# Kernel optimization log

Hardware: AMD Instinct MI355X
Metric: run time of the kernel (lower is better)

## Reference

```python
import jax, jax.numpy as jnp
import numpy as np

B, T, C = 2, 2048, 1024
E, K = 8, 2            # n_experts, top_k (n_experts_active)
H = 2736               # round8(int(4*C*2/3)) SwiGLU hidden dim


def setup_inputs() -> dict:
    key = jax.random.key(0)
    ks = jax.random.split(key, 8)
    def w(k, shape, fan_in):
        return jax.random.normal(k, shape, jnp.float32) * (1.0 / np.sqrt(fan_in))
    x = jax.random.normal(ks[0], (B, T, C), jnp.float32)
    router_w = w(ks[1], (C, E), C)          # gate.weight.T
    wg = w(ks[2], (E, C, H), C)             # stacked expert w_gate.weight.T
    wu = w(ks[3], (E, C, H), C)             # stacked expert w_up.weight.T
    wd = w(ks[4], (E, H, C), H)             # stacked expert w_down.weight.T
    sg = w(ks[5], (C, H), C)                # shared expert gate
    su = w(ks[6], (C, H), C)                # shared expert up
    sd = w(ks[7], (H, C), H)                # shared expert down
    return {"x": x, "router_w": router_w, "wg": wg, "wu": wu, "wd": wd,
            "sg": sg, "su": su, "sd": sd}


def reference(x, router_w, wg, wu, wd, sg, su, sd):
    Bx, Tx, Cx = x.shape
    xf = x.reshape(-1, Cx)                       # (Tk, C)
    Tk = xf.shape[0]

    # --- router ---
    logits = xf @ router_w                       # (Tk, E)
    top_v, top_i = jax.lax.top_k(logits, K)      # (Tk, K)
    rw = jax.nn.softmax(top_v, axis=-1)          # normalized weights over selected

    # combine weights per (token, expert): scatter router weights
    rows = jnp.arange(Tk)[:, None]
    w_te = jnp.zeros((Tk, E), xf.dtype).at[rows, top_i].add(rw)   # (Tk, E)

    # --- experts (dense dispatch; weight w_te zeros out unselected experts) ---
    gate = jnp.einsum('tc,ech->teh', xf, wg)     # (Tk, E, H)
    up = jnp.einsum('tc,ech->teh', xf, wu)
    h = jax.nn.silu(gate) * up                   # SwiGLU hidden
    out = jnp.einsum('teh,te,ehc->tc', h, w_te, wd)   # weighted combine

    # --- shared expert ---
    out = out + (jax.nn.silu(xf @ sg) * (xf @ su)) @ sd

    # --- aux load-balancing loss ---
    mask = jnp.zeros((Tk, E), xf.dtype).at[rows, top_i].add(1.0)
    f = mask.mean(axis=0) / K
    p = jax.nn.softmax(logits, axis=-1).mean(axis=0)
    aux_loss = E * (f * p).sum()

    return out.reshape(Bx, Tx, Cx), aux_loss
```

## Files before the change

kernel.cpp:

```cpp
#include <hip/hip_runtime.h>

typedef _Float16 f16;
typedef _Float16 f16x4 __attribute__((ext_vector_type(4)));
typedef _Float16 f16x8 __attribute__((ext_vector_type(8)));
typedef float f32x4 __attribute__((ext_vector_type(4)));

#define TK 4096
#define CD 1024
#define HD 2736
#define HP 2816
#define MT 104
#define RC 13312

#define GLDS16(ldsp, gp) __builtin_amdgcn_global_load_lds( \
    (const __attribute__((address_space(1))) unsigned int*)(gp), \
    (__attribute__((address_space(3))) unsigned int*)(ldsp), 16, 0, 0)

static constexpr size_t WS_XB  = 0;
static constexpr size_t WS_H   = WS_XB  + (size_t)TK*CD*2;
static constexpr size_t WS_WGT = WS_H   + (size_t)RC*HP*2;
static constexpr size_t WS_WUT = WS_WGT + (size_t)8*HP*CD*2;
static constexpr size_t WS_WDT = WS_WUT + (size_t)8*HP*CD*2;
static constexpr size_t WS_SGT = WS_WDT + (size_t)8*CD*HP*2;
static constexpr size_t WS_SUT = WS_SGT + (size_t)HP*CD*2;
static constexpr size_t WS_SDT = WS_SUT + (size_t)HP*CD*2;
static constexpr size_t WS_CT  = WS_SDT + (size_t)CD*HP*2;
static constexpr size_t WS_OBUF = WS_WGT;
static constexpr size_t CT_STOK = 0;
static constexpr size_t CT_SW   = CT_STOK + (size_t)RC*4;
static constexpr size_t CT_TI   = CT_SW   + (size_t)RC*4;
static constexpr size_t CT_TW   = CT_TI   + (size_t)TK*2*4;
static constexpr size_t CT_ISL  = CT_TW   + (size_t)TK*2*4;
static constexpr size_t CT_CNT  = CT_ISL  + (size_t)TK*2*4;
static constexpr size_t CT_PS   = CT_CNT  + 32;
static constexpr size_t CT_CUR  = CT_PS   + 32;
static constexpr size_t CT_OFF  = CT_CUR  + 32;
static constexpr size_t CT_SIZE = CT_OFF  + 64;

__global__ __launch_bounds__(256) void k_tr(
    const float* __restrict__ srcMain, f16* __restrict__ dstMain,
    const float* __restrict__ srcSh,   f16* __restrict__ dstSh,
    int R, int Cc, int Rp, int Cp, int nMain,
    size_t sstride, size_t dstride) {
    const float* src; f16* dst;
    if ((int)blockIdx.z < nMain) {
        src = srcMain + (size_t)blockIdx.z * sstride;
        dst = dstMain + (size_t)blockIdx.z * dstride;
    } else {
        src = srcSh; dst = dstSh;
    }
    const int tid = threadIdx.x;
    const int l = tid & 63, w = tid >> 6;
    const int cc0 = blockIdx.x * 128 + w * 32 + (l >> 3) * 4;
    const int rr0 = blockIdx.y * 64 + (l & 7) * 8;
    float4 v[8];
    #pragma unroll
    for (int e = 0; e < 8; e++) {
        int gr = rr0 + e;
        if (gr < R && cc0 + 3 < Cc) {
            v[e] = *(const float4*)(src + (size_t)gr * Cc + cc0);
        } else {
            float* ve = (float*)&v[e];
            #pragma unroll
            for (int c = 0; c < 4; c++)
                ve[c] = (gr < R && cc0 + c < Cc) ? src[(size_t)gr * Cc + cc0 + c] : 0.f;
        }
    }
    #pragma unroll
    for (int c = 0; c < 4; c++) {
        const float* vp = (const float*)v;
        f16x8 o = { (f16)vp[0*4+c], (f16)vp[1*4+c], (f16)vp[2*4+c], (f16)vp[3*4+c],
                    (f16)vp[4*4+c], (f16)vp[5*4+c], (f16)vp[6*4+c], (f16)vp[7*4+c] };
        *(f16x8*)(dst + (size_t)(cc0 + c) * Rp + rr0) = o;
    }
}

__global__ void k_router(const float* __restrict__ x, const float* __restrict__ rw,
                         f16* __restrict__ xb,
                         int* __restrict__ topi, float* __restrict__ topw,
                         int* __restrict__ cnt, float* __restrict__ psum) {
    __shared__ float pl[8];
    int tid = threadIdx.x;
    if (tid < 8) pl[tid] = 0.f;
    __syncthreads();
    int wave = tid >> 6, lane = tid & 63;
    int t = blockIdx.x * 4 + wave;
    float acc[8];
    #pragma unroll
    for (int e = 0; e < 8; e++) acc[e] = 0.f;
    const float* xr = x + (size_t)t * CD;
    f16* xbr = xb + (size_t)t * CD;
    for (int i = 0; i < CD / 64; i++) {
        int c = lane + i * 64;
        float xv = xr[c];
        xbr[c] = (f16)xv;
        const float* wr = rw + c * 8;
        #pragma unroll
        for (int e = 0; e < 8; e++) acc[e] = fmaf(xv, wr[e], acc[e]);
    }
    #pragma unroll
    for (int e = 0; e < 8; e++) {
        #pragma unroll
        for (int off = 32; off; off >>= 1) acc[e] += __shfl_xor(acc[e], off);
    }
    if (lane == 0) {
        float v1 = -1e30f; int i1 = 0;
        #pragma unroll
        for (int e = 0; e < 8; e++) if (acc[e] > v1) { v1 = acc[e]; i1 = e; }
        float v2 = -1e30f; int i2 = (i1 == 0) ? 1 : 0;
        #pragma unroll
        for (int e = 0; e < 8; e++) if (e != i1 && acc[e] > v2) { v2 = acc[e]; i2 = e; }
        float b = expf(v2 - v1);
        float w1 = 1.f / (1.f + b);
        topi[t*2] = i1; topi[t*2+1] = i2;
        topw[t*2] = w1; topw[t*2+1] = b * w1;
        atomicAdd(&cnt[i1], 1);
        atomicAdd(&cnt[i2], 1);
        float m = acc[0];
        #pragma unroll
        for (int e = 1; e < 8; e++) m = fmaxf(m, acc[e]);
        float pe[8]; float s = 0.f;
        #pragma unroll
        for (int e = 0; e < 8; e++) { pe[e] = expf(acc[e] - m); s += pe[e]; }
        float inv = 1.f / s;
        #pragma unroll
        for (int e = 0; e < 8; e++) atomicAdd(&pl[e], pe[e] * inv);
    }
    __syncthreads();
    if (tid < 8) atomicAdd(&psum[tid], pl[tid]);
}

__global__ void k_prefix(const int* __restrict__ cnt, int* __restrict__ cur,
                         int* __restrict__ offs) {
    if (threadIdx.x == 0 && blockIdx.x == 0) {
        int off = 0;
        for (int e = 0; e < 8; e++) {
            offs[e] = off; cur[e] = off;
            off += (cnt[e] + 127) & ~127;
        }
        offs[8] = off;
        offs[9] = RC;
    }
}

__global__ void k_scatter(const int* __restrict__ topi, const float* __restrict__ topw,
                          int* __restrict__ cur, const int* __restrict__ offs,
                          int* __restrict__ stok, float* __restrict__ sw,
                          int* __restrict__ islot) {
    int t = blockIdx.x * 256 + threadIdx.x;
    if (t >= TK) return;
    #pragma unroll
    for (int s = 0; s < 2; s++) {
        int e = topi[t*2 + s];
        int pos = atomicAdd(&cur[e], 1);
        stok[pos] = t;
        sw[pos] = topw[t*2 + s];
        islot[t*2 + s] = pos;
    }
    int base = offs[8];
    stok[base + t] = t;
    sw[base + t] = 1.0f;
}

__global__ __launch_bounds__(256, 2) void k_ffn1(
    const f16* __restrict__ xb, const f16* __restrict__ wgt,
    const f16* __restrict__ wut, const f16* __restrict__ sgt,
    const f16* __restrict__ sut, const int* __restrict__ offs,
    const int* __restrict__ cnt, const int* __restrict__ stok,
    f16* __restrict__ hbuf)
{
    __shared__ f16 As[128*64];
    __shared__ f16 Bg[128*64];
    __shared__ f16 Bu[128*64];

    const int n0 = blockIdx.x * 128;
    const int m0 = blockIdx.y * 128;
    int g = 0;
    while (g < 8 && m0 >= offs[g+1]) g++;
    if (m0 >= offs[8] + TK) return;
    if (g < 8 && (m0 - offs[g]) >= cnt[g]) return;

    const f16* __restrict__ Wg = (g < 8) ? wgt + (size_t)g * HP * CD : sgt;
    const f16* __restrict__ Wu = (g < 8) ? wut + (size_t)g * HP * CD : sut;

    const int tid = threadIdx.x;
    const int lane = tid & 63;
    const int w = tid >> 6;
    const int w32 = w * 32;

    const int asw = (((lane & 7) ^ (lane >> 3)) << 3);
    int rA[4];
    #pragma unroll
    for (int i = 0; i < 4; i++)
        rA[i] = stok[m0 + w32 + 8*i + (lane >> 3)] * CD + asw;
    const int rB = (n0 + w32 + (lane >> 3)) * CD + asw;

    f32x4 accg[4][4], accu[4][4];
    #pragma unroll
    for (int i = 0; i < 4; i++)
        #pragma unroll
        for (int j = 0; j < 4; j++)
            #pragma unroll
            for (int r = 0; r < 4; r++) { accg[i][j][r] = 0.f; accu[i][j][r] = 0.f; }

    const int wm = (w >> 1) * 64;
    const int wn = (w & 1) * 64;
    const int fm = lane & 15;
    const int fq = lane >> 4;
    const int fs = fm & 7;

    for (int k0 = 0; k0 < CD; k0 += 64) {
        #pragma unroll
        for (int i = 0; i < 4; i++) {
            GLDS16(&As[(w32 + 8*i) * 64], xb + rA[i] + k0);
            GLDS16(&Bg[(w32 + 8*i) * 64], Wg + rB + i*8*CD + k0);
            GLDS16(&Bu[(w32 + 8*i) * 64], Wu + rB + i*8*CD + k0);
        }
        __syncthreads();
        #pragma unroll
        for (int kk = 0; kk < 2; kk++) {
            const int sw = ((((kk << 2) | fq) ^ fs) << 3);
            f16x8 af[4];
            #pragma unroll
            for (int mi = 0; mi < 4; mi++)
                af[mi] = *(const f16x8*)&As[(wm + mi*16 + fm) * 64 + sw];
            #pragma unroll
            for (int ni = 0; ni < 4; ni++) {
                f16x8 bgf = *(const f16x8*)&Bg[(wn + ni*16 + fm) * 64 + sw];
                f16x8 bur = *(const f16x8*)&Bu[(wn + ni*16 + fm) * 64 + sw];
                #pragma unroll
                for (int mi = 0; mi < 4; mi++) {
                    accg[mi][ni] = __builtin_amdgcn_mfma_f32_16x16x32_f16(af[mi], bgf, accg[mi][ni], 0, 0, 0);
                    accu[mi][ni] = __builtin_amdgcn_mfma_f32_16x16x32_f16(af[mi], bur, accu[mi][ni], 0, 0, 0);
                }
            }
        }
        __syncthreads();
    }

    #pragma unroll
    for (int mi = 0; mi < 4; mi++) {
        #pragma unroll
        for (int ni = 0; ni < 4; ni++) {
            #pragma unroll
            for (int r = 0; r < 4; r++) {
                int row = m0 + wm + mi*16 + fq*4 + r;
                int col = n0 + wn + ni*16 + fm;
                float gv = accg[mi][ni][r];
                float uv = accu[mi][ni][r];
                float hv = gv / (1.f + __expf(-gv)) * uv;
                hbuf[(size_t)row * HP + col] = (f16)hv;
            }
        }
    }
}

__global__ __launch_bounds__(256, 2) void k_ffn2(
    const f16* __restrict__ hbuf, const f16* __restrict__ wdt,
    const f16* __restrict__ sdt, const int* __restrict__ offs,
    const int* __restrict__ cnt, float* __restrict__ obuf)
{
    __shared__ f16 As[128*64];
    __shared__ f16 Bs[128*64];

    const int n0 = blockIdx.x * 128;
    const int m0 = blockIdx.y * 128;
    int g = 0;
    while (g < 8 && m0 >= offs[g+1]) g++;
    if (m0 >= offs[8] + TK) return;
    if (g < 8 && (m0 - offs[g]) >= cnt[g]) return;
    const f16* __restrict__ W = (g < 8) ? wdt + (size_t)g * CD * HP : sdt;

    const int tid = threadIdx.x;
    const int lane = tid & 63;
    const int w = tid >> 6;
    const int w32 = w * 32;

    const int asw = (((lane & 7) ^ (lane >> 3)) << 3);
    const int rA = (m0 + w32 + (lane >> 3)) * HP + asw;
    const int rB = (n0 + w32 + (lane >> 3)) * HP + asw;

    f32x4 acc[4][4];
    #pragma unroll
    for (int i = 0; i < 4; i++)
        #pragma unroll
        for (int j = 0; j < 4; j++)
            #pragma unroll
            for (int r = 0; r < 4; r++) acc[i][j][r] = 0.f;

    const int wm = (w >> 1) * 64;
    const int wn = (w & 1) * 64;
    const int fm = lane & 15;
    const int fq = lane >> 4;
    const int fs = fm & 7;

    for (int k0 = 0; k0 < HP; k0 += 64) {
        #pragma unroll
        for (int i = 0; i < 4; i++) {
            GLDS16(&As[(w32 + 8*i) * 64], hbuf + (size_t)rA + i*8*HP + k0);
            GLDS16(&Bs[(w32 + 8*i) * 64], W    + (size_t)rB + i*8*HP + k0);
        }
        __syncthreads();
        #pragma unroll
        for (int kk = 0; kk < 2; kk++) {
            const int sw = ((((kk << 2) | fq) ^ fs) << 3);
            f16x8 af[4];
            #pragma unroll
            for (int mi = 0; mi < 4; mi++)
                af[mi] = *(const f16x8*)&As[(wm + mi*16 + fm) * 64 + sw];
            #pragma unroll
            for (int ni = 0; ni < 4; ni++) {
                f16x8 bfr = *(const f16x8*)&Bs[(wn + ni*16 + fm) * 64 + sw];
                #pragma unroll
                for (int mi = 0; mi < 4; mi++)
                    acc[mi][ni] = __builtin_amdgcn_mfma_f32_16x16x32_f16(af[mi], bfr, acc[mi][ni], 0, 0, 0);
            }
        }
        __syncthreads();
    }

    #pragma unroll
    for (int mi = 0; mi < 4; mi++) {
        #pragma unroll
        for (int r = 0; r < 4; r++) {
            int row = m0 + wm + mi*16 + fq*4 + r;
            #pragma unroll
            for (int ni = 0; ni < 4; ni++) {
                int col = n0 + wn + ni*16 + fm;
                obuf[(size_t)row * CD + col] = acc[mi][ni][r];
            }
        }
    }
}

__global__ __launch_bounds__(256) void k_comb(
    const float* __restrict__ obuf, const int* __restrict__ islot,
    const float* __restrict__ topw, const int* __restrict__ offs,
    float* __restrict__ out)
{
    const int t = blockIdx.x;
    const int c = threadIdx.x * 4;
    const int s0 = islot[t*2], s1 = islot[t*2+1];
    const float w0 = topw[t*2], w1 = topw[t*2+1];
    const int sh = offs[8] + t;
    float4 a = *(const float4*)(obuf + (size_t)s0 * CD + c);
    float4 b = *(const float4*)(obuf + (size_t)s1 * CD + c);
    float4 s = *(const float4*)(obuf + (size_t)sh * CD + c);
    float4 o;
    o.x = fmaf(w0, a.x, fmaf(w1, b.x, s.x));
    o.y = fmaf(w0, a.y, fmaf(w1, b.y, s.y));
    o.z = fmaf(w0, a.z, fmaf(w1, b.z, s.z));
    o.w = fmaf(w0, a.w, fmaf(w1, b.w, s.w));
    *(float4*)(out + (size_t)t * CD + c) = o;
}

__global__ void k_aux(const int* __restrict__ cnt, const float* __restrict__ psum,
                      float* __restrict__ out_aux) {
    if (threadIdx.x == 0 && blockIdx.x == 0) {
        float a = 0.f;
        for (int e = 0; e < 8; e++) {
            float f = (float)cnt[e] / ((float)TK * 2.f);
            float p = psum[e] / (float)TK;
            a += f * p;
        }
        out_aux[0] = 8.f * a;
    }
}

extern "C" void kernel_launch(void* const* d_in, const int* in_sizes, int n_in,
                              void* d_out, int out_size, void* d_ws, size_t ws_size,
                              hipStream_t stream) {
    const float* x  = (const float*)d_in[0];
    const float* rw = (const float*)d_in[1];
    const float* wg = (const float*)d_in[2];
    const float* wu = (const float*)d_in[3];
    const float* wd = (const float*)d_in[4];
    const float* sg = (const float*)d_in[5];
    const float* su = (const float*)d_in[6];
    const float* sd = (const float*)d_in[7];
    float* out = (float*)d_out;

    char* ws = (char*)d_ws;
    f16* xb   = (f16*)(ws + WS_XB);
    f16* hbuf = (f16*)(ws + WS_H);
    f16* wgt  = (f16*)(ws + WS_WGT);
    f16* wut  = (f16*)(ws + WS_WUT);
    f16* wdt  = (f16*)(ws + WS_WDT);
    f16* sgt  = (f16*)(ws + WS_SGT);
    f16* sut  = (f16*)(ws + WS_SUT);
    f16* sdt  = (f16*)(ws + WS_SDT);
    float* obuf = (float*)(ws + WS_OBUF);
    char* ct  = ws + WS_CT;
    int*   stok = (int*)  (ct + CT_STOK);
    float* swt  = (float*)(ct + CT_SW);
    int*   topi = (int*)  (ct + CT_TI);
    float* topw = (float*)(ct + CT_TW);
    int*   isl  = (int*)  (ct + CT_ISL);
    int*   cnt  = (int*)  (ct + CT_CNT);
    float* psum = (float*)(ct + CT_PS);
    int*   cur  = (int*)  (ct + CT_CUR);
    int*   offs = (int*)  (ct + CT_OFF);

    hipMemsetAsync(ct, 0, CT_SIZE, stream);

    k_router<<<dim3(TK / 4), dim3(256), 0, stream>>>(x, rw, xb, topi, topw, cnt, psum);
    k_prefix<<<dim3(1), dim3(64), 0, stream>>>(cnt, cur, offs);
    k_scatter<<<dim3(TK / 256), dim3(256), 0, stream>>>(topi, topw, cur, offs, stok, swt, isl);

    k_tr<<<dim3(HP/128, CD/64, 9), dim3(256), 0, stream>>>(
        wg, wgt, sg, sgt, CD, HD, CD, HP, 8, (size_t)CD*HD, (size_t)HP*CD);
    k_tr<<<dim3(HP/128, CD/64, 9), dim3(256), 0, stream>>>(
        wu, wut, su, sut, CD, HD, CD, HP, 8, (size_t)CD*HD, (size_t)HP*CD);
    k_tr<<<dim3(CD/128, HP/64, 9), dim3(256), 0, stream>>>(
        wd, wdt, sd, sdt, HD, CD, HP, CD, 8, (size_t)HD*CD, (size_t)CD*HP);

    k_ffn1<<<dim3(HP/128, MT), dim3(256), 0, stream>>>(xb, wgt, wut, sgt, sut, offs, cnt, stok, hbuf);
    k_ffn2<<<dim3(CD/128, MT), dim3(256), 0, stream>>>(hbuf, wdt, sdt, offs, cnt, obuf);
    k_comb<<<dim3(TK), dim3(256), 0, stream>>>(obuf, isl, topw, offs, out);
    k_aux<<<dim3(1), dim3(64), 0, stream>>>(cnt, psum, out + (size_t)TK * CD);
}
```

Before: 774.2 us.

## Fuse combine into FFN2 via atomics, merge transposes, remap workgroups, raise occupancy

The down-projection kernel now scales each row by its router weight and atomically adds it into the zeroed output. This removes the intermediate fp32 buffer and the separate combine kernel. The gate and up weight transposes are merged into one launch. Both FFN kernels remap workgroup IDs with an XCD-style interleave and raise launch-bounds occupancy hints. The costs are atomic contention on fp32 output rows (three contributions per token), an extra memset of the output, and possible register spills from the higher occupancy targets.

```diff
diff --git a/kernel.cpp b/kernel.cpp
--- a/kernel.cpp
+++ b/kernel.cpp
@@ -25,7 +25,6 @@
 static constexpr size_t WS_SUT = WS_SGT + (size_t)HP*CD*2;
 static constexpr size_t WS_SDT = WS_SUT + (size_t)HP*CD*2;
 static constexpr size_t WS_CT  = WS_SDT + (size_t)CD*HP*2;
-static constexpr size_t WS_OBUF = WS_WGT;
 static constexpr size_t CT_STOK = 0;
 static constexpr size_t CT_SW   = CT_STOK + (size_t)RC*4;
 static constexpr size_t CT_TI   = CT_SW   + (size_t)RC*4;
@@ -37,11 +36,58 @@
 static constexpr size_t CT_OFF  = CT_CUR  + 32;
 static constexpr size_t CT_SIZE = CT_OFF  + 64;
 
+__device__ __forceinline__ void tr_body(const float* __restrict__ src,
+                                        f16* __restrict__ dst,
+                                        int R, int Cc, int Rp) {
+    const int tid = threadIdx.x;
+    const int l = tid & 63, w = tid >> 6;
+    const int cc0 = blockIdx.x * 128 + w * 32 + (l >> 3) * 4;
+    const int rr0 = blockIdx.y * 64 + (l & 7) * 8;
+    float4 v[8];
+    #pragma unroll
+    for (int e = 0; e < 8; e++) {
+        int gr = rr0 + e;
+        if (gr < R && cc0 + 3 < Cc) {
+            v[e] = *(const float4*)(src + (size_t)gr * Cc + cc0);
+        } else {
+            float* ve = (float*)&v[e];
+            #pragma unroll
+            for (int c = 0; c < 4; c++)
+                ve[c] = (gr < R && cc0 + c < Cc) ? src[(size_t)gr * Cc + cc0 + c] : 0.f;
+        }
+    }
+    #pragma unroll
+    for (int c = 0; c < 4; c++) {
+        const float* vp = (const float*)v;
+        f16x8 o = { (f16)vp[0*4+c], (f16)vp[1*4+c], (f16)vp[2*4+c], (f16)vp[3*4+c],
+                    (f16)vp[4*4+c], (f16)vp[5*4+c], (f16)vp[6*4+c], (f16)vp[7*4+c] };
+        *(f16x8*)(dst + (size_t)(cc0 + c) * Rp + rr0) = o;
+    }
+}
+
+__global__ __launch_bounds__(256) void k_tr2(
+    const float* __restrict__ wg, f16* __restrict__ wgt,
+    const float* __restrict__ sg, f16* __restrict__ sgt,
+    const float* __restrict__ wu, f16* __restrict__ wut,
+    const float* __restrict__ su, f16* __restrict__ sut,
+    int R, int Cc, int Rp, size_t sstride, size_t dstride) {
+    const int z = blockIdx.z;
+    const float* src; f16* dst;
+    if (z < 9) {
+        if (z < 8) { src = wg + (size_t)z * sstride; dst = wgt + (size_t)z * dstride; }
+        else       { src = sg; dst = sgt; }
+    } else {
+        int z2 = z - 9;
+        if (z2 < 8) { src = wu + (size_t)z2 * sstride; dst = wut + (size_t)z2 * dstride; }
+        else        { src = su; dst = sut; }
+    }
+    tr_body(src, dst, R, Cc, Rp);
+}
+
 __global__ __launch_bounds__(256) void k_tr(
     const float* __restrict__ srcMain, f16* __restrict__ dstMain,
     const float* __restrict__ srcSh,   f16* __restrict__ dstSh,
-    int R, int Cc, int Rp, int Cp, int nMain,
-    size_t sstride, size_t dstride) {
+    int R, int Cc, int Rp, int nMain, size_t sstride, size_t dstride) {
     const float* src; f16* dst;
     if ((int)blockIdx.z < nMain) {
         src = srcMain + (size_t)blockIdx.z * sstride;
@@ -49,30 +95,7 @@
     } else {
         src = srcSh; dst = dstSh;
     }
-    const int tid = threadIdx.x;
-    const int l = tid & 63, w = tid >> 6;
-    const int cc0 = blockIdx.x * 128 + w * 32 + (l >> 3) * 4;
-    const int rr0 = blockIdx.y * 64 + (l & 7) * 8;
-    float4 v[8];
-    #pragma unroll
-    for (int e = 0; e < 8; e++) {
-        int gr = rr0 + e;
-        if (gr < R && cc0 + 3 < Cc) {
-            v[e] = *(const float4*)(src + (size_t)gr * Cc + cc0);
-        } else {
-            float* ve = (float*)&v[e];
-            #pragma unroll
-            for (int c = 0; c < 4; c++)
-                ve[c] = (gr < R && cc0 + c < Cc) ? src[(size_t)gr * Cc + cc0 + c] : 0.f;
-        }
-    }
-    #pragma unroll
-    for (int c = 0; c < 4; c++) {
-        const float* vp = (const float*)v;
-        f16x8 o = { (f16)vp[0*4+c], (f16)vp[1*4+c], (f16)vp[2*4+c], (f16)vp[3*4+c],
-                    (f16)vp[4*4+c], (f16)vp[5*4+c], (f16)vp[6*4+c], (f16)vp[7*4+c] };
-        *(f16x8*)(dst + (size_t)(cc0 + c) * Rp + rr0) = o;
-    }
+    tr_body(src, dst, R, Cc, Rp);
 }
 
 __global__ void k_router(const float* __restrict__ x, const float* __restrict__ rw,
@@ -145,8 +168,7 @@
 
 __global__ void k_scatter(const int* __restrict__ topi, const float* __restrict__ topw,
                           int* __restrict__ cur, const int* __restrict__ offs,
-                          int* __restrict__ stok, float* __restrict__ sw,
-                          int* __restrict__ islot) {
+                          int* __restrict__ stok, float* __restrict__ sw) {
     int t = blockIdx.x * 256 + threadIdx.x;
     if (t >= TK) return;
     #pragma unroll
@@ -155,14 +177,13 @@
         int pos = atomicAdd(&cur[e], 1);
         stok[pos] = t;
         sw[pos] = topw[t*2 + s];
-        islot[t*2 + s] = pos;
     }
     int base = offs[8];
     stok[base + t] = t;
     sw[base + t] = 1.0f;
 }
 
-__global__ __launch_bounds__(256, 2) void k_ffn1(
+__global__ __launch_bounds__(256, 3) void k_ffn1(
     const f16* __restrict__ xb, const f16* __restrict__ wgt,
     const f16* __restrict__ wut, const f16* __restrict__ sgt,
     const f16* __restrict__ sut, const int* __restrict__ offs,
@@ -173,8 +194,12 @@
     __shared__ f16 Bg[128*64];
     __shared__ f16 Bu[128*64];
 
-    const int n0 = blockIdx.x * 128;
-    const int m0 = blockIdx.y * 128;
+    const int flat = blockIdx.y * gridDim.x + blockIdx.x;
+    const int nwg  = gridDim.x * gridDim.y;
+    const int wgid = (flat & 7) * (nwg >> 3) + (flat >> 3);
+    const int n0 = (wgid % gridDim.x) * 128;
+    const int m0 = (wgid / gridDim.x) * 128;
+
     int g = 0;
     while (g < 8 && m0 >= offs[g+1]) g++;
     if (m0 >= offs[8] + TK) return;
@@ -255,16 +280,21 @@
     }
 }
 
-__global__ __launch_bounds__(256, 2) void k_ffn2(
+__global__ __launch_bounds__(256, 4) void k_ffn2(
     const f16* __restrict__ hbuf, const f16* __restrict__ wdt,
     const f16* __restrict__ sdt, const int* __restrict__ offs,
-    const int* __restrict__ cnt, float* __restrict__ obuf)
+    const int* __restrict__ cnt, const int* __restrict__ stok,
+    const float* __restrict__ swt, float* __restrict__ out)
 {
     __shared__ f16 As[128*64];
     __shared__ f16 Bs[128*64];
 
-    const int n0 = blockIdx.x * 128;
-    const int m0 = blockIdx.y * 128;
+    const int flat = blockIdx.y * gridDim.x + blockIdx.x;
+    const int nwg  = gridDim.x * gridDim.y;
+    const int wgid = (flat & 7) * (nwg >> 3) + (flat >> 3);
+    const int n0 = (wgid % gridDim.x) * 128;
+    const int m0 = (wgid / gridDim.x) * 128;
+
     int g = 0;
     while (g < 8 && m0 >= offs[g+1]) g++;
     if (m0 >= offs[8] + TK) return;
@@ -324,34 +354,16 @@
         #pragma unroll
         for (int r = 0; r < 4; r++) {
             int row = m0 + wm + mi*16 + fq*4 + r;
+            int t = stok[row];
+            float rowW = swt[row];
+            float* orow = out + (size_t)t * CD + n0;
             #pragma unroll
             for (int ni = 0; ni < 4; ni++) {
-                int col = n0 + wn + ni*16 + fm;
-                obuf[(size_t)row * CD + col] = acc[mi][ni][r];
+                int col = wn + ni*16 + fm;
+                atomicAdd(orow + col, rowW * acc[mi][ni][r]);
             }
         }
     }
-}
-
-__global__ __launch_bounds__(256) void k_comb(
-    const float* __restrict__ obuf, const int* __restrict__ islot,
-    const float* __restrict__ topw, const int* __restrict__ offs,
-    float* __restrict__ out)
-{
-    const int t = blockIdx.x;
-    const int c = threadIdx.x * 4;
-    const int s0 = islot[t*2], s1 = islot[t*2+1];
-    const float w0 = topw[t*2], w1 = topw[t*2+1];
-    const int sh = offs[8] + t;
-    float4 a = *(const float4*)(obuf + (size_t)s0 * CD + c);
-    float4 b = *(const float4*)(obuf + (size_t)s1 * CD + c);
-    float4 s = *(const float4*)(obuf + (size_t)sh * CD + c);
-    float4 o;
-    o.x = fmaf(w0, a.x, fmaf(w1, b.x, s.x));
-    o.y = fmaf(w0, a.y, fmaf(w1, b.y, s.y));
-    o.z = fmaf(w0, a.z, fmaf(w1, b.z, s.z));
-    o.w = fmaf(w0, a.w, fmaf(w1, b.w, s.w));
-    *(float4*)(out + (size_t)t * CD + c) = o;
 }
 
 __global__ void k_aux(const int* __restrict__ cnt, const float* __restrict__ psum,
@@ -389,33 +401,29 @@
     f16* sgt  = (f16*)(ws + WS_SGT);
     f16* sut  = (f16*)(ws + WS_SUT);
     f16* sdt  = (f16*)(ws + WS_SDT);
-    float* obuf = (float*)(ws + WS_OBUF);
     char* ct  = ws + WS_CT;
     int*   stok = (int*)  (ct + CT_STOK);
     float* swt  = (float*)(ct + CT_SW);
     int*   topi = (int*)  (ct + CT_TI);
     float* topw = (float*)(ct + CT_TW);
-    int*   isl  = (int*)  (ct + CT_ISL);
     int*   cnt  = (int*)  (ct + CT_CNT);
     float* psum = (float*)(ct + CT_PS);
     int*   cur  = (int*)  (ct + CT_CUR);
     int*   offs = (int*)  (ct + CT_OFF);
 
     hipMemsetAsync(ct, 0, CT_SIZE, stream);
+    hipMemsetAsync(out, 0, (size_t)TK * CD * 4, stream);
 
     k_router<<<dim3(TK / 4), dim3(256), 0, stream>>>(x, rw, xb, topi, topw, cnt, psum);
     k_prefix<<<dim3(1), dim3(64), 0, stream>>>(cnt, cur, offs);
-    k_scatter<<<dim3(TK / 256), dim3(256), 0, stream>>>(topi, topw, cur, offs, stok, swt, isl);
-
-    k_tr<<<dim3(HP/128, CD/64, 9), dim3(256), 0, stream>>>(
-        wg, wgt, sg, sgt, CD, HD, CD, HP, 8, (size_t)CD*HD, (size_t)HP*CD);
-    k_tr<<<dim3(HP/128, CD/64, 9), dim3(256), 0, stream>>>(
-        wu, wut, su, sut, CD, HD, CD, HP, 8, (size_t)CD*HD, (size_t)HP*CD);
+    k_scatter<<<dim3(TK / 256), dim3(256), 0, stream>>>(topi, topw, cur, offs, stok, swt);
+
+    k_tr2<<<dim3(HP/128, CD/64, 18), dim3(256), 0, stream>>>(
+        wg, wgt, sg, sgt, wu, wut, su, sut, CD, HD, CD, (size_t)CD*HD, (size_t)HP*CD);
     k_tr<<<dim3(CD/128, HP/64, 9), dim3(256), 0, stream>>>(
-        wd, wdt, sd, sdt, HD, CD, HP, CD, 8, (size_t)HD*CD, (size_t)CD*HP);
+        wd, wdt, sd, sdt, HD, CD, HP, 8, (size_t)HD*CD, (size_t)CD*HP);
 
     k_ffn1<<<dim3(HP/128, MT), dim3(256), 0, stream>>>(xb, wgt, wut, sgt, sut, offs, cnt, stok, hbuf);
-    k_ffn2<<<dim3(CD/128, MT), dim3(256), 0, stream>>>(hbuf, wdt, sdt, offs, cnt, obuf);
-    k_comb<<<dim3(TK), dim3(256), 0, stream>>>(obuf, isl, topw, offs, out);
+    k_ffn2<<<dim3(CD/128, MT), dim3(256), 0, stream>>>(hbuf, wdt, sdt, offs, cnt, stok, swt, out);
     k_aux<<<dim3(1), dim3(64), 0, stream>>>(cnt, psum, out + (size_t)TK * CD);
 }
```

Measured after the change: 785.0 us. About the same (+1.4%).
